# Kernel optimization log

Hardware: AMD Instinct MI355X
Metric: run time of the kernel (lower is better)

Reference implementation:

```python
import jax, jax.numpy as jnp
import numpy as np

# binarize = sign() in forward; standard BNN binarize uses a straight-through
# estimator (gradient clipped to |x|<=1) in backward. Forward math: sign.

def binarize(x):
    return jnp.sign(x)


def setup_inputs() -> dict:
    key = jax.random.key(0)
    k1, k2 = jax.random.split(key)
    M, K, N = 8192, 4096, 4096
    x = jax.random.normal(k1, (M, K), dtype=jnp.float32)
    # xavier-scale init for weight; scale is irrelevant after sign() but kept realistic
    w = jax.random.normal(k2, (K, N), dtype=jnp.float32) * np.sqrt(2.0 / (K + N)).astype(np.float32)
    return {"x": x, "weight": w}


def reference(x, weight):
    # sign-binarize activations and weights, then dense matmul
    xb = binarize(x)            # [M, K] in {-1, 0, +1}
    wb = binarize(weight)       # [K, N]
    return jnp.matmul(xb, wb)   # [M, N]
```

## Files before the change

kernel.cpp:

```cpp
#include <hip/hip_runtime.h>
#include <stdint.h>

#define M_DIM 8192
#define K_DIM 4096
#define N_DIM 4096

using i32x4 = __attribute__((ext_vector_type(4))) int;
using i32x8 = __attribute__((ext_vector_type(8))) int;
using f32x16 = __attribute__((ext_vector_type(16))) float;

typedef const __attribute__((address_space(1))) void g_void;
typedef __attribute__((address_space(3))) void lds_void;

__device__ __forceinline__ void gload_lds16(const void* g, void* l) {
  __builtin_amdgcn_global_load_lds((g_void*)g, (lds_void*)l, 16, 0, 0);
}

__device__ __forceinline__ void barrier_raw() {
  asm volatile("" ::: "memory");
  __builtin_amdgcn_s_barrier();
  asm volatile("" ::: "memory");
}

__device__ __forceinline__ unsigned code4(float v) {
  return v > 0.f ? 0x2u : (v < 0.f ? 0xAu : 0x0u);
}

__global__ void pack_x4_kernel(const float* __restrict__ in,
                               uint8_t* __restrict__ out) {
  __shared__ __align__(16) uint16_t cds[32 * 264];
  int g = blockIdx.x;
  int tq = blockIdx.y;
  int tid = threadIdx.x;
#pragma unroll
  for (int i = 0; i < 32; ++i) {
    int flat = tid + 256 * i;
    int row = flat >> 8;
    int c4 = flat & 255;
    const float4 v = *reinterpret_cast<const float4*>(
        in + (long)(g * 32 + row) * K_DIM + tq * 1024 + c4 * 4);
    unsigned u = code4(v.x) | (code4(v.y) << 4) | (code4(v.z) << 8) |
                 (code4(v.w) << 12);
    cds[row * 264 + c4] = (uint16_t)u;
  }
  __syncthreads();
#pragma unroll
  for (int j = 0; j < 4; ++j) {
    int u = tid + 256 * j;
    int tl = u >> 7;
    int kc = (u >> 5) & 3;
    int row = u & 31;
    i32x4 val = *reinterpret_cast<const i32x4*>(
        &cds[row * 264 + tl * 32 + kc * 8]);
    int t = tq * 8 + tl;
    long o = ((((long)g * 32 + t) * 4 + kc) * 32 + row) * 16;
    *reinterpret_cast<i32x4*>(out + o) = val;
  }
}

__global__ void pack_wt4_kernel(const float* __restrict__ w,
                                uint8_t* __restrict__ out) {
  __shared__ __align__(16) uint8_t tile[64 * 144];
  int n0 = blockIdx.x * 64;
  int k0 = blockIdx.y * 128;
  int tid = threadIdx.x;
#pragma unroll
  for (int i = 0; i < 32; ++i) {
    int flat = tid + 256 * i;
    int r = flat >> 6;
    int c = flat & 63;
    tile[c * 144 + r] = (uint8_t)code4(w[(long)(k0 + r) * N_DIM + n0 + c]);
  }
  __syncthreads();
  int rg = tid >> 7, kc = (tid >> 5) & 3, row = tid & 31;
  const unsigned* sp =
      reinterpret_cast<const unsigned*>(&tile[(rg * 32 + row) * 144 + kc * 32]);
  i32x4 val;
#pragma unroll
  for (int d = 0; d < 4; ++d) {
    unsigned s0 = sp[2 * d], s1 = sp[2 * d + 1];
    unsigned t0 = s0 & 0x0F0F0F0Fu, t1 = s1 & 0x0F0F0F0Fu;
    unsigned p = (t0 | (t0 >> 4)) & 0x00FF00FFu;
    unsigned q = (t1 | (t1 >> 4)) & 0x00FF00FFu;
    val[d] = (int)((p & 0xFFu) | ((p >> 8) & 0xFF00u) | ((q & 0xFFu) << 16) |
                   ((q >> 16) << 24));
  }
  int g = (n0 >> 5) + rg;
  int t = k0 >> 7;
  long o = ((((long)g * 32 + t) * 4 + kc) * 32 + row) * 16;
  *reinterpret_cast<i32x4*>(out + o) = val;
}

__device__ __forceinline__ i32x8 lo8(i32x4 r) {
  return __builtin_shufflevector(r, r, 0, 1, 2, 3, -1, -1, -1, -1);
}

#define SCALE1 0x7f7f7f7f

template <int VM, bool ISSUE>
__device__ __forceinline__ void tile_step(
    int t, const uint8_t* __restrict__ gA, const uint8_t* __restrict__ gB,
    int dstA, int dstB, uint8_t* lds, int aRd, int bRd, f32x16 (&acc)[4][2]) {
  const uint8_t* buf = lds + (t & 3) * 32768;
  if (ISSUE) {
    long kn = (long)(t + 3) * 2048;
    uint8_t* nbuf = lds + ((t + 3) & 3) * 32768;
    gload_lds16(gA + kn, nbuf + dstA);
    gload_lds16(gA + kn + 1024, nbuf + dstA + 1024);
    gload_lds16(gB + kn, nbuf + dstB);
    gload_lds16(gB + kn + 1024, nbuf + dstB + 1024);
  }
  i32x4 a0[4], b0[2], a1[4], b1[2];
#pragma unroll
  for (int mi = 0; mi < 4; ++mi)
    a0[mi] = *reinterpret_cast<const i32x4*>(buf + aRd + mi * 2048);
#pragma unroll
  for (int ni = 0; ni < 2; ++ni)
    b0[ni] = *reinterpret_cast<const i32x4*>(buf + bRd + ni * 2048);
#pragma unroll
  for (int mi = 0; mi < 4; ++mi)
    a1[mi] = *reinterpret_cast<const i32x4*>(buf + aRd + mi * 2048 + 1024);
#pragma unroll
  for (int ni = 0; ni < 2; ++ni)
    b1[ni] = *reinterpret_cast<const i32x4*>(buf + bRd + ni * 2048 + 1024);
  asm volatile("s_waitcnt lgkmcnt(6)" ::: "memory");
  __builtin_amdgcn_sched_barrier(0);
  __builtin_amdgcn_s_setprio(1);
#pragma unroll
  for (int mi = 0; mi < 4; ++mi)
#pragma unroll
    for (int ni = 0; ni < 2; ++ni)
      acc[mi][ni] = __builtin_amdgcn_mfma_scale_f32_32x32x64_f8f6f4(
          lo8(a0[mi]), lo8(b0[ni]), acc[mi][ni], 4, 4, 0, SCALE1, 0, SCALE1);
  __builtin_amdgcn_s_setprio(0);
  asm volatile("s_waitcnt lgkmcnt(0)" ::: "memory");
  __builtin_amdgcn_sched_barrier(0);
  __builtin_amdgcn_s_setprio(1);
#pragma unroll
  for (int mi = 0; mi < 4; ++mi)
#pragma unroll
    for (int ni = 0; ni < 2; ++ni)
      acc[mi][ni] = __builtin_amdgcn_mfma_scale_f32_32x32x64_f8f6f4(
          lo8(a1[mi]), lo8(b1[ni]), acc[mi][ni], 4, 4, 0, SCALE1, 0, SCALE1);
  __builtin_amdgcn_s_setprio(0);
  if (VM >= 0) {
    if (VM == 8) asm volatile("s_waitcnt vmcnt(8)" ::: "memory");
    else if (VM == 4) asm volatile("s_waitcnt vmcnt(4)" ::: "memory");
    else asm volatile("s_waitcnt vmcnt(0)" ::: "memory");
    barrier_raw();
  }
}

__global__ __launch_bounds__(512, 2) void gemm_fp4_kernel(
    const uint8_t* __restrict__ A, const uint8_t* __restrict__ B,
    float* __restrict__ C) {
  __shared__ __align__(16) uint8_t lds[4 * 32768];

  int bid = blockIdx.x;
  int xcd = bid & 7;
  int i = bid >> 3;
  int bn = (i & 7) + ((xcd & 1) << 3);
  int bm = (i >> 3) + ((xcd >> 1) << 3);

  int tid = threadIdx.x;
  int wid = tid >> 6;
  int lane = tid & 63;
  int wr = wid >> 2;
  int wc = wid & 3;

  const uint8_t* gA = A + (long)(bm * 8 + wid) * 32 * 2048 + lane * 16;
  const uint8_t* gB = B + (long)(bn * 8 + wid) * 32 * 2048 + lane * 16;
  int dstA = wid * 2048;
  int dstB = 16384 + wid * 2048;

  int aRd = (wr * 4) * 2048 + lane * 16;
  int bRd = 16384 + (wc * 2) * 2048 + lane * 16;

  f32x16 acc[4][2] = {};

#pragma unroll
  for (int t = 0; t < 3; ++t) {
    uint8_t* buf = lds + t * 32768;
    long k0 = (long)t * 2048;
    gload_lds16(gA + k0, buf + dstA);
    gload_lds16(gA + k0 + 1024, buf + dstA + 1024);
    gload_lds16(gB + k0, buf + dstB);
    gload_lds16(gB + k0 + 1024, buf + dstB + 1024);
  }
  asm volatile("s_waitcnt vmcnt(8)" ::: "memory");
  barrier_raw();

#pragma unroll 1
  for (int t = 0; t < 29; ++t)
    tile_step<8, true>(t, gA, gB, dstA, dstB, lds, aRd, bRd, acc);
  tile_step<4, false>(29, gA, gB, dstA, dstB, lds, aRd, bRd, acc);
  tile_step<0, false>(30, gA, gB, dstA, dstB, lds, aRd, bRd, acc);
  tile_step<-1, false>(31, gA, gB, dstA, dstB, lds, aRd, bRd, acc);

  long row0 = (long)bm * 256 + wr * 128 + ((lane >> 5) << 2);
  long col0 = (long)bn * 256 + wc * 64 + (lane & 31);
#pragma unroll
  for (int mi = 0; mi < 4; ++mi)
#pragma unroll
    for (int ni = 0; ni < 2; ++ni)
#pragma unroll
      for (int r = 0; r < 16; ++r) {
        long row = row0 + mi * 32 + (r & 3) + ((r >> 2) << 3);
        C[row * N_DIM + col0 + ni * 32] = acc[mi][ni][r];
      }
}

extern "C" void kernel_launch(void* const* d_in, const int* in_sizes, int n_in,
                              void* d_out, int out_size, void* d_ws, size_t ws_size,
                              hipStream_t stream) {
  const float* x = (const float*)d_in[0];
  const float* w = (const float*)d_in[1];
  float* out = (float*)d_out;

  uint8_t* x4 = (uint8_t*)d_ws;
  uint8_t* w4t = x4 + (size_t)M_DIM * (K_DIM / 2);

  pack_x4_kernel<<<dim3(M_DIM / 32, 4), 256, 0, stream>>>(x, x4);
  pack_wt4_kernel<<<dim3(N_DIM / 64, K_DIM / 128), 256, 0, stream>>>(w, w4t);
  gemm_fp4_kernel<<<512, 512, 0, stream>>>(x4, w4t, out);
}
```

Before: 132.1 us.

## Prefetch next K-tile LDS fragments into registers during current MFMA step

Restructures the main loop into a register double-buffered software pipeline. Each step runs the first half of its MFMAs on fragments already in registers, then waits on the barrier and issues the global-to-LDS prefetch. It then starts LDS reads for the next tile while the second MFMA half executes. This hides LDS read latency behind matrix math, at the cost of doubling the fragment registers and tightening vmcnt/lgkmcnt bookkeeping, which could hurt occupancy or correctness if the counts are off.

```diff
diff --git a/kernel.cpp b/kernel.cpp
--- a/kernel.cpp
+++ b/kernel.cpp
@@ -50,8 +50,7 @@
     int tl = u >> 7;
     int kc = (u >> 5) & 3;
     int row = u & 31;
-    i32x4 val = *reinterpret_cast<const i32x4*>(
-        &cds[row * 264 + tl * 32 + kc * 8]);
+    i32x4 val = *reinterpret_cast<const i32x4*>(&cds[row * 264 + tl * 32 + kc * 8]);
     int t = tq * 8 + tl;
     long o = ((((long)g * 32 + t) * 4 + kc) * 32 + row) * 16;
     *reinterpret_cast<i32x4*>(out + o) = val;
@@ -97,11 +96,26 @@
 
 #define SCALE1 0x7f7f7f7f
 
-template <int VM, bool ISSUE>
+template <int VM, bool ISSUE, bool READ>
 __device__ __forceinline__ void tile_step(
     int t, const uint8_t* __restrict__ gA, const uint8_t* __restrict__ gB,
-    int dstA, int dstB, uint8_t* lds, int aRd, int bRd, f32x16 (&acc)[4][2]) {
-  const uint8_t* buf = lds + (t & 3) * 32768;
+    int dstA, int dstB, uint8_t* lds, int aRd, int bRd, i32x4 (&aC)[8],
+    i32x4 (&bC)[4], i32x4 (&aN)[8], i32x4 (&bN)[4], f32x16 (&acc)[4][2]) {
+  asm volatile("s_waitcnt lgkmcnt(6)" ::: "memory");
+  __builtin_amdgcn_sched_barrier(0);
+  __builtin_amdgcn_s_setprio(1);
+#pragma unroll
+  for (int mi = 0; mi < 4; ++mi)
+#pragma unroll
+    for (int ni = 0; ni < 2; ++ni)
+      acc[mi][ni] = __builtin_amdgcn_mfma_scale_f32_32x32x64_f8f6f4(
+          lo8(aC[mi]), lo8(bC[ni]), acc[mi][ni], 4, 4, 0, SCALE1, 0, SCALE1);
+  __builtin_amdgcn_s_setprio(0);
+  if (VM >= 0) {
+    if (VM == 4) asm volatile("s_waitcnt vmcnt(4)" ::: "memory");
+    else asm volatile("s_waitcnt vmcnt(0)" ::: "memory");
+    barrier_raw();
+  }
   if (ISSUE) {
     long kn = (long)(t + 3) * 2048;
     uint8_t* nbuf = lds + ((t + 3) & 3) * 32768;
@@ -110,20 +124,25 @@
     gload_lds16(gB + kn, nbuf + dstB);
     gload_lds16(gB + kn + 1024, nbuf + dstB + 1024);
   }
-  i32x4 a0[4], b0[2], a1[4], b1[2];
-#pragma unroll
-  for (int mi = 0; mi < 4; ++mi)
-    a0[mi] = *reinterpret_cast<const i32x4*>(buf + aRd + mi * 2048);
-#pragma unroll
-  for (int ni = 0; ni < 2; ++ni)
-    b0[ni] = *reinterpret_cast<const i32x4*>(buf + bRd + ni * 2048);
-#pragma unroll
-  for (int mi = 0; mi < 4; ++mi)
-    a1[mi] = *reinterpret_cast<const i32x4*>(buf + aRd + mi * 2048 + 1024);
-#pragma unroll
-  for (int ni = 0; ni < 2; ++ni)
-    b1[ni] = *reinterpret_cast<const i32x4*>(buf + bRd + ni * 2048 + 1024);
-  asm volatile("s_waitcnt lgkmcnt(6)" ::: "memory");
+  if (READ) {
+    const uint8_t* nb = lds + ((t + 1) & 3) * 32768;
+#pragma unroll
+    for (int mi = 0; mi < 4; ++mi)
+      aN[mi] = *reinterpret_cast<const i32x4*>(nb + aRd + mi * 2048);
+#pragma unroll
+    for (int ni = 0; ni < 2; ++ni)
+      bN[ni] = *reinterpret_cast<const i32x4*>(nb + bRd + ni * 2048);
+#pragma unroll
+    for (int mi = 0; mi < 4; ++mi)
+      aN[4 + mi] = *reinterpret_cast<const i32x4*>(nb + aRd + mi * 2048 + 1024);
+#pragma unroll
+    for (int ni = 0; ni < 2; ++ni)
+      bN[2 + ni] = *reinterpret_cast<const i32x4*>(nb + bRd + ni * 2048 + 1024);
+  }
+  if (READ)
+    asm volatile("s_waitcnt lgkmcnt(12)" ::: "memory");
+  else
+    asm volatile("s_waitcnt lgkmcnt(0)" ::: "memory");
   __builtin_amdgcn_sched_barrier(0);
   __builtin_amdgcn_s_setprio(1);
 #pragma unroll
@@ -131,24 +150,9 @@
 #pragma unroll
     for (int ni = 0; ni < 2; ++ni)
       acc[mi][ni] = __builtin_amdgcn_mfma_scale_f32_32x32x64_f8f6f4(
-          lo8(a0[mi]), lo8(b0[ni]), acc[mi][ni], 4, 4, 0, SCALE1, 0, SCALE1);
+          lo8(aC[4 + mi]), lo8(bC[2 + ni]), acc[mi][ni], 4, 4, 0, SCALE1, 0,
+          SCALE1);
   __builtin_amdgcn_s_setprio(0);
-  asm volatile("s_waitcnt lgkmcnt(0)" ::: "memory");
-  __builtin_amdgcn_sched_barrier(0);
-  __builtin_amdgcn_s_setprio(1);
-#pragma unroll
-  for (int mi = 0; mi < 4; ++mi)
-#pragma unroll
-    for (int ni = 0; ni < 2; ++ni)
-      acc[mi][ni] = __builtin_amdgcn_mfma_scale_f32_32x32x64_f8f6f4(
-          lo8(a1[mi]), lo8(b1[ni]), acc[mi][ni], 4, 4, 0, SCALE1, 0, SCALE1);
-  __builtin_amdgcn_s_setprio(0);
-  if (VM >= 0) {
-    if (VM == 8) asm volatile("s_waitcnt vmcnt(8)" ::: "memory");
-    else if (VM == 4) asm volatile("s_waitcnt vmcnt(4)" ::: "memory");
-    else asm volatile("s_waitcnt vmcnt(0)" ::: "memory");
-    barrier_raw();
-  }
 }
 
 __global__ __launch_bounds__(512, 2) void gemm_fp4_kernel(
@@ -176,6 +180,7 @@
   int aRd = (wr * 4) * 2048 + lane * 16;
   int bRd = 16384 + (wc * 2) * 2048 + lane * 16;
 
+  i32x4 aA[8], bA[4], aB[8], bB[4];
   f32x16 acc[4][2] = {};
 
 #pragma unroll
@@ -189,13 +194,34 @@
   }
   asm volatile("s_waitcnt vmcnt(8)" ::: "memory");
   barrier_raw();
+#pragma unroll
+  for (int mi = 0; mi < 4; ++mi)
+    aA[mi] = *reinterpret_cast<const i32x4*>(lds + aRd + mi * 2048);
+#pragma unroll
+  for (int ni = 0; ni < 2; ++ni)
+    bA[ni] = *reinterpret_cast<const i32x4*>(lds + bRd + ni * 2048);
+#pragma unroll
+  for (int mi = 0; mi < 4; ++mi)
+    aA[4 + mi] = *reinterpret_cast<const i32x4*>(lds + aRd + mi * 2048 + 1024);
+#pragma unroll
+  for (int ni = 0; ni < 2; ++ni)
+    bA[2 + ni] = *reinterpret_cast<const i32x4*>(lds + bRd + ni * 2048 + 1024);
 
 #pragma unroll 1
-  for (int t = 0; t < 29; ++t)
-    tile_step<8, true>(t, gA, gB, dstA, dstB, lds, aRd, bRd, acc);
-  tile_step<4, false>(29, gA, gB, dstA, dstB, lds, aRd, bRd, acc);
-  tile_step<0, false>(30, gA, gB, dstA, dstB, lds, aRd, bRd, acc);
-  tile_step<-1, false>(31, gA, gB, dstA, dstB, lds, aRd, bRd, acc);
+  for (int t = 0; t < 28; t += 2) {
+    tile_step<4, true, true>(t, gA, gB, dstA, dstB, lds, aRd, bRd, aA, bA, aB,
+                             bB, acc);
+    tile_step<4, true, true>(t + 1, gA, gB, dstA, dstB, lds, aRd, bRd, aB, bB,
+                             aA, bA, acc);
+  }
+  tile_step<4, true, true>(28, gA, gB, dstA, dstB, lds, aRd, bRd, aA, bA, aB,
+                           bB, acc);
+  tile_step<4, false, true>(29, gA, gB, dstA, dstB, lds, aRd, bRd, aB, bB, aA,
+                            bA, acc);
+  tile_step<0, false, true>(30, gA, gB, dstA, dstB, lds, aRd, bRd, aA, bA, aB,
+                            bB, acc);
+  tile_step<-1, false, false>(31, gA, gB, dstA, dstB, lds, aRd, bRd, aB, bB,
+                              aA, bA, acc);
 
   long row0 = (long)bm * 256 + wr * 128 + ((lane >> 5) << 2);
   long col0 = (long)bn * 256 + wc * 64 + (lane & 31);
```

After: 131.1 us. No clear change (-0.7%).

## Shrink GEMM block tile to 128x256 with 4 waves and 3-stage pipeline

Applied to the files above, without the earlier changes.

The fp4 GEMM block tile goes from 256x256 with 8 waves to 128x256 with 4 waves, launching 1024 blocks of 256 threads instead of 512 of 512. The LDS pipeline drops from 4 stages of 32KB to 3 stages of 24KB, with the stage index made compile-time by unrolling the main loop by 3. Each wave now loads two B slabs per k-tile, and the vmcnt waits are adjusted to match. The aim is more blocks per CU and cheaper LDS addressing, at the cost of less A/B reuse per block and a shallower prefetch depth.

```diff
diff --git a/kernel.cpp b/kernel.cpp
--- a/kernel.cpp
+++ b/kernel.cpp
@@ -50,8 +50,7 @@
     int tl = u >> 7;
     int kc = (u >> 5) & 3;
     int row = u & 31;
-    i32x4 val = *reinterpret_cast<const i32x4*>(
-        &cds[row * 264 + tl * 32 + kc * 8]);
+    i32x4 val = *reinterpret_cast<const i32x4*>(&cds[row * 264 + tl * 32 + kc * 8]);
     int t = tq * 8 + tl;
     long o = ((((long)g * 32 + t) * 4 + kc) * 32 + row) * 16;
     *reinterpret_cast<i32x4*>(out + o) = val;
@@ -97,18 +96,22 @@
 
 #define SCALE1 0x7f7f7f7f
 
-template <int VM, bool ISSUE>
+template <int VM, bool ISSUE, int CUR>
 __device__ __forceinline__ void tile_step(
-    int t, const uint8_t* __restrict__ gA, const uint8_t* __restrict__ gB,
-    int dstA, int dstB, uint8_t* lds, int aRd, int bRd, f32x16 (&acc)[4][2]) {
-  const uint8_t* buf = lds + (t & 3) * 32768;
+    int t, const uint8_t* __restrict__ gA, const uint8_t* __restrict__ gB0,
+    const uint8_t* __restrict__ gB1, int dstA, int dstB, uint8_t* lds,
+    int aRd, int bRd, f32x16 (&acc)[4][2]) {
+  const uint8_t* buf = lds + CUR * 24576;
+  constexpr int SN = (CUR + 2) % 3;
   if (ISSUE) {
-    long kn = (long)(t + 3) * 2048;
-    uint8_t* nbuf = lds + ((t + 3) & 3) * 32768;
+    long kn = (long)(t + 2) * 2048;
+    uint8_t* nbuf = lds + SN * 24576;
     gload_lds16(gA + kn, nbuf + dstA);
     gload_lds16(gA + kn + 1024, nbuf + dstA + 1024);
-    gload_lds16(gB + kn, nbuf + dstB);
-    gload_lds16(gB + kn + 1024, nbuf + dstB + 1024);
+    gload_lds16(gB0 + kn, nbuf + dstB);
+    gload_lds16(gB0 + kn + 1024, nbuf + dstB + 1024);
+    gload_lds16(gB1 + kn, nbuf + dstB + 2048);
+    gload_lds16(gB1 + kn + 1024, nbuf + dstB + 3072);
   }
   i32x4 a0[4], b0[2], a1[4], b1[2];
 #pragma unroll
@@ -144,61 +147,63 @@
           lo8(a1[mi]), lo8(b1[ni]), acc[mi][ni], 4, 4, 0, SCALE1, 0, SCALE1);
   __builtin_amdgcn_s_setprio(0);
   if (VM >= 0) {
-    if (VM == 8) asm volatile("s_waitcnt vmcnt(8)" ::: "memory");
-    else if (VM == 4) asm volatile("s_waitcnt vmcnt(4)" ::: "memory");
+    if (VM == 6) asm volatile("s_waitcnt vmcnt(6)" ::: "memory");
     else asm volatile("s_waitcnt vmcnt(0)" ::: "memory");
     barrier_raw();
   }
 }
 
-__global__ __launch_bounds__(512, 2) void gemm_fp4_kernel(
+__global__ __launch_bounds__(256, 2) void gemm_fp4_kernel(
     const uint8_t* __restrict__ A, const uint8_t* __restrict__ B,
     float* __restrict__ C) {
-  __shared__ __align__(16) uint8_t lds[4 * 32768];
+  __shared__ __align__(16) uint8_t lds[3 * 24576];
 
   int bid = blockIdx.x;
   int xcd = bid & 7;
   int i = bid >> 3;
   int bn = (i & 7) + ((xcd & 1) << 3);
-  int bm = (i >> 3) + ((xcd >> 1) << 3);
+  int bm = (i >> 3) + ((xcd >> 1) << 4);
 
   int tid = threadIdx.x;
   int wid = tid >> 6;
   int lane = tid & 63;
-  int wr = wid >> 2;
-  int wc = wid & 3;
-
-  const uint8_t* gA = A + (long)(bm * 8 + wid) * 32 * 2048 + lane * 16;
-  const uint8_t* gB = B + (long)(bn * 8 + wid) * 32 * 2048 + lane * 16;
+
+  const uint8_t* gA = A + (long)(bm * 4 + wid) * 65536 + lane * 16;
+  const uint8_t* gB0 = B + (long)(bn * 8 + 2 * wid) * 65536 + lane * 16;
+  const uint8_t* gB1 = gB0 + 65536;
   int dstA = wid * 2048;
-  int dstB = 16384 + wid * 2048;
-
-  int aRd = (wr * 4) * 2048 + lane * 16;
-  int bRd = 16384 + (wc * 2) * 2048 + lane * 16;
+  int dstB = 8192 + wid * 4096;
+
+  int aRd = lane * 16;
+  int bRd = 8192 + (wid * 2) * 2048 + lane * 16;
 
   f32x16 acc[4][2] = {};
 
 #pragma unroll
-  for (int t = 0; t < 3; ++t) {
-    uint8_t* buf = lds + t * 32768;
+  for (int t = 0; t < 2; ++t) {
+    uint8_t* buf = lds + t * 24576;
     long k0 = (long)t * 2048;
     gload_lds16(gA + k0, buf + dstA);
     gload_lds16(gA + k0 + 1024, buf + dstA + 1024);
-    gload_lds16(gB + k0, buf + dstB);
-    gload_lds16(gB + k0 + 1024, buf + dstB + 1024);
-  }
-  asm volatile("s_waitcnt vmcnt(8)" ::: "memory");
+    gload_lds16(gB0 + k0, buf + dstB);
+    gload_lds16(gB0 + k0 + 1024, buf + dstB + 1024);
+    gload_lds16(gB1 + k0, buf + dstB + 2048);
+    gload_lds16(gB1 + k0 + 1024, buf + dstB + 3072);
+  }
+  asm volatile("s_waitcnt vmcnt(6)" ::: "memory");
   barrier_raw();
 
 #pragma unroll 1
-  for (int t = 0; t < 29; ++t)
-    tile_step<8, true>(t, gA, gB, dstA, dstB, lds, aRd, bRd, acc);
-  tile_step<4, false>(29, gA, gB, dstA, dstB, lds, aRd, bRd, acc);
-  tile_step<0, false>(30, gA, gB, dstA, dstB, lds, aRd, bRd, acc);
-  tile_step<-1, false>(31, gA, gB, dstA, dstB, lds, aRd, bRd, acc);
-
-  long row0 = (long)bm * 256 + wr * 128 + ((lane >> 5) << 2);
-  long col0 = (long)bn * 256 + wc * 64 + (lane & 31);
+  for (int tt = 0; tt < 30; tt += 3) {
+    tile_step<6, true, 0>(tt, gA, gB0, gB1, dstA, dstB, lds, aRd, bRd, acc);
+    tile_step<6, true, 1>(tt + 1, gA, gB0, gB1, dstA, dstB, lds, aRd, bRd, acc);
+    tile_step<6, true, 2>(tt + 2, gA, gB0, gB1, dstA, dstB, lds, aRd, bRd, acc);
+  }
+  tile_step<0, false, 0>(30, gA, gB0, gB1, dstA, dstB, lds, aRd, bRd, acc);
+  tile_step<-1, false, 1>(31, gA, gB0, gB1, dstA, dstB, lds, aRd, bRd, acc);
+
+  long row0 = (long)bm * 128 + ((lane >> 5) << 2);
+  long col0 = (long)bn * 256 + wid * 64 + (lane & 31);
 #pragma unroll
   for (int mi = 0; mi < 4; ++mi)
 #pragma unroll
@@ -222,5 +227,5 @@
 
   pack_x4_kernel<<<dim3(M_DIM / 32, 4), 256, 0, stream>>>(x, x4);
   pack_wt4_kernel<<<dim3(N_DIM / 64, K_DIM / 128), 256, 0, stream>>>(w, w4t);
-  gemm_fp4_kernel<<<512, 512, 0, stream>>>(x4, w4t, out);
-}
+  gemm_fp4_kernel<<<1024, 256, 0, stream>>>(x4, w4t, out);
+}
```

Result: faster. 124.4 us, median of 2 (-5.8%).
